# Optimization experiments

Hardware: AMD Instinct MI355X
Metric: run time of the kernel (lower is better)

The kernel has to match this reference:

```python
import jax, jax.numpy as jnp
import numpy as np

N_NODES = 100000
N_EDGES = 1600000
IN_CH = 64
HEADS = 8
OUT_CH = 16
NEG_SLOPE = 0.2  # PyG GATConv default


def setup_inputs() -> dict:
    key = jax.random.key(0)
    ks = jax.random.split(key, 6)
    x = jax.random.normal(ks[0], (N_NODES, IN_CH), dtype=jnp.float32)
    edge_index = jax.random.randint(ks[1], (2, N_EDGES), 0, N_NODES, dtype=jnp.int32)
    # learned parameters (PyG GATConv: shared lin for src/dst, att vectors, bias for concat output)
    W = jax.random.normal(ks[2], (HEADS * OUT_CH, IN_CH), dtype=jnp.float32) / np.sqrt(IN_CH)
    att_src = jax.random.normal(ks[3], (HEADS, OUT_CH), dtype=jnp.float32) / np.sqrt(OUT_CH)
    att_dst = jax.random.normal(ks[4], (HEADS, OUT_CH), dtype=jnp.float32) / np.sqrt(OUT_CH)
    bias = jax.random.normal(ks[5], (HEADS * OUT_CH,), dtype=jnp.float32) * 0.01
    return {"x": x, "edge_index": edge_index, "W": W,
            "att_src": att_src, "att_dst": att_dst, "bias": bias}


def reference(x, edge_index, W, att_src, att_dst, bias):
    n = x.shape[0]
    # linear projection -> [N, H, C]
    h = (x @ W.T).reshape(n, HEADS, OUT_CH)
    # per-node halves of the attention logit
    a_src = jnp.einsum('nhc,hc->nh', h, att_src)  # [N, H]
    a_dst = jnp.einsum('nhc,hc->nh', h, att_dst)  # [N, H]
    # add self loops (PyG default add_self_loops=True)
    loops = jnp.arange(n, dtype=edge_index.dtype)
    src = jnp.concatenate([edge_index[0], loops])
    dst = jnp.concatenate([edge_index[1], loops])
    # edge attention: leaky_relu then segment-softmax over incoming edges of dst
    e = jax.nn.leaky_relu(a_src[src] + a_dst[dst], NEG_SLOPE)  # [E+N, H]
    e_max = jax.ops.segment_max(e, dst, num_segments=n)
    e = jnp.exp(e - e_max[dst])
    denom = jax.ops.segment_sum(e, dst, num_segments=n)
    alpha = e / (denom[dst] + 1e-16)  # [E+N, H]
    # weighted scatter-add aggregation
    msg = h[src] * alpha[:, :, None]  # [E+N, H, C]
    out = jax.ops.segment_sum(msg, dst, num_segments=n).reshape(n, HEADS * OUT_CH)
    out = out + bias
    # unlinear: act='relu', norm=None
    return jax.nn.relu(out)
```

## Files before the change

### kernel.cpp

```cpp
#include <hip/hip_runtime.h>

#define N_NODESC 100000
#define N_EDGESC 1600000
#define HCC 128
#define E_TOTC (N_EDGESC + N_NODESC)
#define SCAN_NB 391
#define PROJ_NB 1563
#define POS_NB 831

using short8 = __attribute__((ext_vector_type(8))) short;
using f32x4  = __attribute__((ext_vector_type(4))) float;

__device__ __forceinline__ float lrelu(float v) { return fmaxf(v, 0.2f * v); }
__device__ __forceinline__ unsigned short f2bf(float f) {
    unsigned u = __float_as_uint(f);
    unsigned r = ((u >> 16) & 1u) + 0x7fffu;
    return (unsigned short)((u + r) >> 16);
}
__device__ __forceinline__ short8 pack8(float4 a, float4 b) {
    short8 v;
    v[0] = (short)f2bf(a.x); v[1] = (short)f2bf(a.y);
    v[2] = (short)f2bf(a.z); v[3] = (short)f2bf(a.w);
    v[4] = (short)f2bf(b.x); v[5] = (short)f2bf(b.y);
    v[6] = (short)f2bf(b.z); v[7] = (short)f2bf(b.w);
    return v;
}

__launch_bounds__(256, 4)
__global__ void proj_pos_kernel(const float* __restrict__ x, const float* __restrict__ W,
                                const float* __restrict__ att_src, const float* __restrict__ att_dst,
                                unsigned short* __restrict__ h16,
                                float* __restrict__ a_src, float* __restrict__ a_dst,
                                const int* __restrict__ ei, int* __restrict__ deg,
                                int* __restrict__ posb) {
    const int t = threadIdx.x;

    if (blockIdx.x >= PROJ_NB) {
        const int e0 = (blockIdx.x - PROJ_NB) * 2048 + t;
#pragma unroll
        for (int j = 0; j < 8; ++j) {
            int e = e0 + 256 * j;
            if (e < E_TOTC) {
                int d = (e < N_EDGESC) ? ei[N_EDGESC + e] : (e - N_EDGESC);
                posb[e] = atomicAdd(&deg[d], 1);
            }
        }
        return;
    }

    const int l  = t & 63;
    const int lc = l & 15;
    const int lg = l >> 4;
    const int row0 = blockIdx.x * 64 + (t >> 6) * 16;
    const int rA = min(row0 + lc, N_NODESC - 1);

    f32x4 acc[8];
#pragma unroll
    for (int i = 0; i < 8; ++i) acc[i] = (f32x4){0.f, 0.f, 0.f, 0.f};

#pragma unroll
    for (int s = 0; s < 2; ++s) {
        const float4* xp = (const float4*)(x + (size_t)rA * 64 + s * 32 + lg * 8);
        float4 x0 = xp[0], x1 = xp[1];
        short8 af = pack8(x0, x1);
#pragma unroll
        for (int t2 = 0; t2 < 8; ++t2) {
            const float4* wp = (const float4*)(W + (size_t)(t2 * 16 + lc) * 64 + s * 32 + lg * 8);
            float4 w0 = wp[0], w1 = wp[1];
            short8 bf = pack8(w0, w1);
            acc[t2] = __builtin_amdgcn_mfma_f32_16x16x32_bf16(af, bf, acc[t2], 0, 0, 0);
        }
    }

#pragma unroll
    for (int hd = 0; hd < 8; ++hd) {
        const float as_ = att_src[hd * 16 + lc];
        const float ad_ = att_dst[hd * 16 + lc];
#pragma unroll
        for (int j = 0; j < 4; ++j) {
            const int grow = row0 + lg * 4 + j;
            const float hv = acc[hd][j];
            float ts = hv * as_;
            float td = hv * ad_;
            ts += __shfl_xor(ts, 1); ts += __shfl_xor(ts, 2);
            ts += __shfl_xor(ts, 4); ts += __shfl_xor(ts, 8);
            td += __shfl_xor(td, 1); td += __shfl_xor(td, 2);
            td += __shfl_xor(td, 4); td += __shfl_xor(td, 8);
            if (grow < N_NODESC) {
                h16[(size_t)grow * HCC + hd * 16 + lc] = f2bf(hv);
                if (lc == 0) {
                    a_src[(size_t)grow * 8 + hd] = ts;
                    a_dst[(size_t)grow * 8 + hd] = td;
                }
            }
        }
    }
}

__global__ void scan1_kernel(const int* __restrict__ deg, int* __restrict__ bsum) {
    __shared__ int lds[256];
    int i = blockIdx.x * 256 + threadIdx.x;
    lds[threadIdx.x] = (i < N_NODESC) ? deg[i] : 0;
    __syncthreads();
    for (int off = 128; off > 0; off >>= 1) {
        if (threadIdx.x < off) lds[threadIdx.x] += lds[threadIdx.x + off];
        __syncthreads();
    }
    if (threadIdx.x == 0) bsum[blockIdx.x] = lds[0];
}

__global__ void scan2_kernel(int* __restrict__ bsum) {
    __shared__ int lds[512];
    int t = threadIdx.x;
    lds[t] = (t < SCAN_NB) ? bsum[t] : 0;
    __syncthreads();
    for (int off = 1; off < 512; off <<= 1) {
        int u = 0;
        if (t >= off) u = lds[t - off];
        __syncthreads();
        if (t >= off) lds[t] += u;
        __syncthreads();
    }
    if (t < SCAN_NB) bsum[t] = (t == 0) ? 0 : lds[t - 1];
}

__global__ void scan3_kernel(const int* __restrict__ deg, const int* __restrict__ bsum,
                             int* __restrict__ rowptr) {
    __shared__ int lds[256];
    int t = threadIdx.x;
    int i = blockIdx.x * 256 + t;
    int v = (i < N_NODESC) ? deg[i] : 0;
    lds[t] = v;
    __syncthreads();
    for (int off = 1; off < 256; off <<= 1) {
        int u = 0;
        if (t >= off) u = lds[t - off];
        __syncthreads();
        if (t >= off) lds[t] += u;
        __syncthreads();
    }
    int excl = bsum[blockIdx.x] + lds[t] - v;
    if (i < N_NODESC) rowptr[i] = excl;
    if (i == 0) rowptr[N_NODESC] = E_TOTC;
}

__global__ void scatter_kernel(const int* __restrict__ ei, const int* __restrict__ rowptr,
                               const int* __restrict__ posb, int* __restrict__ colsrc) {
    int e = blockIdx.x * 256 + threadIdx.x;
    if (e >= E_TOTC) return;
    int s, d;
    if (e < N_EDGESC) { s = ei[e]; d = ei[N_EDGESC + e]; }
    else              { s = d = e - N_EDGESC; }
    colsrc[rowptr[d] + posb[e]] = s;
}

__launch_bounds__(256, 8)
__global__ void agg_csr_kernel(const int* __restrict__ rowptr, const int* __restrict__ colsrc,
                               const float* __restrict__ a_src, const float* __restrict__ a_dst,
                               const unsigned* __restrict__ h32,
                               const float* __restrict__ bias, float* __restrict__ out) {
    const int t = threadIdx.x;
    const int L = t & 63;
    const int n = blockIdx.x * 4 + (t >> 6);
    const int hd = L >> 3;
    const int eL = L & 7;

    const int beg = rowptr[n], end = rowptr[n + 1];
    const float ad = a_dst[n * 8 + hd];

    float den = 0.f;
    float acc[16];
#pragma unroll
    for (int j = 0; j < 16; ++j) acc[j] = 0.f;

    int p = beg + eL;
    bool vld = p < end;
    int s = vld ? colsrc[p] : 0;
    float av = vld ? a_src[s * 8 + hd] : 0.f;

    while (vld) {
        const uint4* hp = (const uint4*)(h32 + (size_t)s * 64 + hd * 8);
        const uint4 ha = hp[0];
        const uint4 hb = hp[1];
        const int p2 = p + 8;
        const bool v2 = p2 < end;
        const int s2 = v2 ? colsrc[p2] : 0;
        const float av2 = v2 ? a_src[s2 * 8 + hd] : 0.f;

        const float pr = __expf(lrelu(av + ad));
        den += pr;
        acc[0]  = fmaf(pr, __uint_as_float(ha.x << 16),         acc[0]);
        acc[1]  = fmaf(pr, __uint_as_float(ha.x & 0xffff0000u), acc[1]);
        acc[2]  = fmaf(pr, __uint_as_float(ha.y << 16),         acc[2]);
        acc[3]  = fmaf(pr, __uint_as_float(ha.y & 0xffff0000u), acc[3]);
        acc[4]  = fmaf(pr, __uint_as_float(ha.z << 16),         acc[4]);
        acc[5]  = fmaf(pr, __uint_as_float(ha.z & 0xffff0000u), acc[5]);
        acc[6]  = fmaf(pr, __uint_as_float(ha.w << 16),         acc[6]);
        acc[7]  = fmaf(pr, __uint_as_float(ha.w & 0xffff0000u), acc[7]);
        acc[8]  = fmaf(pr, __uint_as_float(hb.x << 16),         acc[8]);
        acc[9]  = fmaf(pr, __uint_as_float(hb.x & 0xffff0000u), acc[9]);
        acc[10] = fmaf(pr, __uint_as_float(hb.y << 16),         acc[10]);
        acc[11] = fmaf(pr, __uint_as_float(hb.y & 0xffff0000u), acc[11]);
        acc[12] = fmaf(pr, __uint_as_float(hb.z << 16),         acc[12]);
        acc[13] = fmaf(pr, __uint_as_float(hb.z & 0xffff0000u), acc[13]);
        acc[14] = fmaf(pr, __uint_as_float(hb.w << 16),         acc[14]);
        acc[15] = fmaf(pr, __uint_as_float(hb.w & 0xffff0000u), acc[15]);

        p = p2; s = s2; av = av2; vld = v2;
    }

    den += __shfl_xor(den, 1); den += __shfl_xor(den, 2); den += __shfl_xor(den, 4);
#pragma unroll
    for (int j = 0; j < 16; ++j) {
        acc[j] += __shfl_xor(acc[j], 1);
        acc[j] += __shfl_xor(acc[j], 2);
        acc[j] += __shfl_xor(acc[j], 4);
    }
    const float inv = 1.f / (den + 1e-16f);
    float ox = acc[0], oy = acc[1];
#pragma unroll
    for (int j = 1; j < 8; ++j) {
        ox = (eL == j) ? acc[2 * j]     : ox;
        oy = (eL == j) ? acc[2 * j + 1] : oy;
    }
    const float2 b = ((const float2*)bias)[L];
    float2 o;
    o.x = fmaxf(ox * inv + b.x, 0.f);
    o.y = fmaxf(oy * inv + b.y, 0.f);
    ((float2*)out)[(size_t)n * 64 + L] = o;
}

extern "C" void kernel_launch(void* const* d_in, const int* in_sizes, int n_in,
                              void* d_out, int out_size, void* d_ws, size_t ws_size,
                              hipStream_t stream) {
    const float* x       = (const float*)d_in[0];
    const int*   ei      = (const int*)d_in[1];
    const float* W       = (const float*)d_in[2];
    const float* att_src = (const float*)d_in[3];
    const float* att_dst = (const float*)d_in[4];
    const float* bias    = (const float*)d_in[5];
    float* out = (float*)d_out;

    float* ws    = (float*)d_ws;
    unsigned short* h16 = (unsigned short*)ws;
    float* a_src = ws + 6400000;
    float* a_dst = a_src + 800000;
    int* deg     = (int*)(a_dst + 800000);
    int* rowptr  = deg + 100000;
    int* bsum    = rowptr + 100001;
    int* posb    = bsum + 512;
    int* colsrc  = posb + 1700000;

    hipMemsetAsync(deg, 0, 100000 * sizeof(int), stream);

    proj_pos_kernel<<<PROJ_NB + POS_NB, 256, 0, stream>>>(x, W, att_src, att_dst,
                                                          h16, a_src, a_dst,
                                                          ei, deg, posb);
    scan1_kernel<<<SCAN_NB, 256, 0, stream>>>(deg, bsum);
    scan2_kernel<<<1, 512, 0, stream>>>(bsum);
    scan3_kernel<<<SCAN_NB, 256, 0, stream>>>(deg, bsum, rowptr);
    scatter_kernel<<<(E_TOTC + 255) / 256, 256, 0, stream>>>(ei, rowptr, posb, colsrc);

    agg_csr_kernel<<<N_NODESC / 4, 256, 0, stream>>>(rowptr, colsrc, a_src, a_dst,
                                                     (const unsigned*)h16, bias, out);
}
```

Measured before the change: 226.0 us.

## Replace bf16 MFMA projection with fp32 LDS-tiled GEMM and folded attention vectors

The fused MFMA projection and edge-position kernel is split into three kernels: a small prep kernel that transposes W and folds att_src/att_dst into W to give per-input-channel attention weights, an fp32 LDS-tiled register-blocked projection kernel that computes h and both attention logits directly, and a separate position/atomic kernel. This removes the shuffle reductions and the bf16 rounding of inputs, which improves precision. In exchange it uses fp32 FMA instead of matrix cores, adds two kernel launches, and gives up the overlap between projection and the atomic degree count.

```diff
diff --git a/kernel.cpp b/kernel.cpp
--- a/kernel.cpp
+++ b/kernel.cpp
@@ -5,11 +5,7 @@
 #define HCC 128
 #define E_TOTC (N_EDGESC + N_NODESC)
 #define SCAN_NB 391
-#define PROJ_NB 1563
-#define POS_NB 831
-
-using short8 = __attribute__((ext_vector_type(8))) short;
-using f32x4  = __attribute__((ext_vector_type(4))) float;
+#define PROJ_NB 782
 
 __device__ __forceinline__ float lrelu(float v) { return fmaxf(v, 0.2f * v); }
 __device__ __forceinline__ unsigned short f2bf(float f) {
@@ -17,84 +13,107 @@
     unsigned r = ((u >> 16) & 1u) + 0x7fffu;
     return (unsigned short)((u + r) >> 16);
 }
-__device__ __forceinline__ short8 pack8(float4 a, float4 b) {
-    short8 v;
-    v[0] = (short)f2bf(a.x); v[1] = (short)f2bf(a.y);
-    v[2] = (short)f2bf(a.z); v[3] = (short)f2bf(a.w);
-    v[4] = (short)f2bf(b.x); v[5] = (short)f2bf(b.y);
-    v[6] = (short)f2bf(b.z); v[7] = (short)f2bf(b.w);
-    return v;
-}
-
-__launch_bounds__(256, 4)
-__global__ void proj_pos_kernel(const float* __restrict__ x, const float* __restrict__ W,
-                                const float* __restrict__ att_src, const float* __restrict__ att_dst,
-                                unsigned short* __restrict__ h16,
-                                float* __restrict__ a_src, float* __restrict__ a_dst,
-                                const int* __restrict__ ei, int* __restrict__ deg,
-                                int* __restrict__ posb) {
+
+__global__ void wu_kernel(const float* __restrict__ W,
+                          const float* __restrict__ att_src, const float* __restrict__ att_dst,
+                          float* __restrict__ WT, float* __restrict__ us_g) {
+    int t = blockIdx.x * 256 + threadIdx.x;
+    if (t < 8192) {
+        int k = t >> 7, c = t & 127;
+        WT[t] = W[c * 64 + k];
+    } else {
+        int o = t - 8192;
+        int k = o >> 4, c = o & 15;
+        const int h = (c < 8) ? c : c - 8;
+        const float* av = (c < 8) ? att_src : att_dst;
+        float s = 0.f;
+#pragma unroll
+        for (int j = 0; j < 16; ++j) s += av[h * 16 + j] * W[(h * 16 + j) * 64 + k];
+        us_g[o] = s;
+    }
+}
+
+__launch_bounds__(256, 2)
+__global__ void proj_kernel(const float* __restrict__ x, const float* __restrict__ WT,
+                            const float* __restrict__ us_g,
+                            unsigned short* __restrict__ h16,
+                            float* __restrict__ a_src, float* __restrict__ a_dst) {
+    __shared__ float xs[128][68];
+    __shared__ float ws[64][132];
+    __shared__ float us[64][16];
     const int t = threadIdx.x;
-
-    if (blockIdx.x >= PROJ_NB) {
-        const int e0 = (blockIdx.x - PROJ_NB) * 2048 + t;
-#pragma unroll
-        for (int j = 0; j < 8; ++j) {
-            int e = e0 + 256 * j;
-            if (e < E_TOTC) {
-                int d = (e < N_EDGESC) ? ei[N_EDGESC + e] : (e - N_EDGESC);
-                posb[e] = atomicAdd(&deg[d], 1);
-            }
+    const int row0 = blockIdx.x * 128;
+
+    const float4* wt4 = (const float4*)WT;
+    float4* ws4 = (float4*)&ws[0][0];
+#pragma unroll
+    for (int j = 0; j < 8; ++j) {
+        int q = t + 256 * j;
+        int k = q >> 5, c4 = q & 31;
+        *(float4*)&ws[k][c4 * 4] = wt4[q];
+    }
+    ((float4*)&us[0][0])[t] = ((const float4*)us_g)[t];
+
+#pragma unroll
+    for (int j = 0; j < 8; ++j) {
+        int f = (t + 256 * j) * 4;
+        int r = f >> 6, k = f & 63;
+        int gr = row0 + r;
+        if (gr >= N_NODESC) gr = N_NODESC - 1;
+        float4 v = *(const float4*)&x[(size_t)gr * 64 + k];
+        *(float4*)&xs[r][k] = v;
+    }
+    __syncthreads();
+
+    const int rg = t & 15;
+    const int cg = t >> 4;
+    float acc[8][8], acca[8];
+#pragma unroll
+    for (int i = 0; i < 8; ++i) {
+        acca[i] = 0.f;
+#pragma unroll
+        for (int j = 0; j < 8; ++j) acc[i][j] = 0.f;
+    }
+
+#pragma unroll 4
+    for (int k = 0; k < 64; ++k) {
+        float xv[8];
+#pragma unroll
+        for (int i = 0; i < 8; ++i) xv[i] = xs[rg + 16 * i][k];
+        float4 w0 = *(const float4*)&ws[k][4 * cg];
+        float4 w1 = *(const float4*)&ws[k][64 + 4 * cg];
+        float uv = us[k][cg];
+#pragma unroll
+        for (int i = 0; i < 8; ++i) {
+            acc[i][0] += xv[i] * w0.x; acc[i][1] += xv[i] * w0.y;
+            acc[i][2] += xv[i] * w0.z; acc[i][3] += xv[i] * w0.w;
+            acc[i][4] += xv[i] * w1.x; acc[i][5] += xv[i] * w1.y;
+            acc[i][6] += xv[i] * w1.z; acc[i][7] += xv[i] * w1.w;
+            acca[i]   += xv[i] * uv;
         }
-        return;
-    }
-
-    const int l  = t & 63;
-    const int lc = l & 15;
-    const int lg = l >> 4;
-    const int row0 = blockIdx.x * 64 + (t >> 6) * 16;
-    const int rA = min(row0 + lc, N_NODESC - 1);
-
-    f32x4 acc[8];
-#pragma unroll
-    for (int i = 0; i < 8; ++i) acc[i] = (f32x4){0.f, 0.f, 0.f, 0.f};
-
-#pragma unroll
-    for (int s = 0; s < 2; ++s) {
-        const float4* xp = (const float4*)(x + (size_t)rA * 64 + s * 32 + lg * 8);
-        float4 x0 = xp[0], x1 = xp[1];
-        short8 af = pack8(x0, x1);
-#pragma unroll
-        for (int t2 = 0; t2 < 8; ++t2) {
-            const float4* wp = (const float4*)(W + (size_t)(t2 * 16 + lc) * 64 + s * 32 + lg * 8);
-            float4 w0 = wp[0], w1 = wp[1];
-            short8 bf = pack8(w0, w1);
-            acc[t2] = __builtin_amdgcn_mfma_f32_16x16x32_bf16(af, bf, acc[t2], 0, 0, 0);
+    }
+
+#pragma unroll
+    for (int i = 0; i < 8; ++i) {
+        int gr = row0 + rg + 16 * i;
+        if (gr < N_NODESC) {
+            ushort4 p0, p1;
+            p0.x = f2bf(acc[i][0]); p0.y = f2bf(acc[i][1]); p0.z = f2bf(acc[i][2]); p0.w = f2bf(acc[i][3]);
+            p1.x = f2bf(acc[i][4]); p1.y = f2bf(acc[i][5]); p1.z = f2bf(acc[i][6]); p1.w = f2bf(acc[i][7]);
+            *(ushort4*)&h16[(size_t)gr * HCC + 4 * cg] = p0;
+            *(ushort4*)&h16[(size_t)gr * HCC + 64 + 4 * cg] = p1;
+            if (cg < 8) a_src[(size_t)gr * 8 + cg] = acca[i];
+            else        a_dst[(size_t)gr * 8 + cg - 8] = acca[i];
         }
     }
-
-#pragma unroll
-    for (int hd = 0; hd < 8; ++hd) {
-        const float as_ = att_src[hd * 16 + lc];
-        const float ad_ = att_dst[hd * 16 + lc];
-#pragma unroll
-        for (int j = 0; j < 4; ++j) {
-            const int grow = row0 + lg * 4 + j;
-            const float hv = acc[hd][j];
-            float ts = hv * as_;
-            float td = hv * ad_;
-            ts += __shfl_xor(ts, 1); ts += __shfl_xor(ts, 2);
-            ts += __shfl_xor(ts, 4); ts += __shfl_xor(ts, 8);
-            td += __shfl_xor(td, 1); td += __shfl_xor(td, 2);
-            td += __shfl_xor(td, 4); td += __shfl_xor(td, 8);
-            if (grow < N_NODESC) {
-                h16[(size_t)grow * HCC + hd * 16 + lc] = f2bf(hv);
-                if (lc == 0) {
-                    a_src[(size_t)grow * 8 + hd] = ts;
-                    a_dst[(size_t)grow * 8 + hd] = td;
-                }
-            }
-        }
-    }
+}
+
+__global__ void pos_kernel(const int* __restrict__ ei, int* __restrict__ deg,
+                           int* __restrict__ posb) {
+    int e = blockIdx.x * 256 + threadIdx.x;
+    if (e >= E_TOTC) return;
+    int d = (e < N_EDGESC) ? ei[N_EDGESC + e] : (e - N_EDGESC);
+    posb[e] = atomicAdd(&deg[d], 1);
 }
 
 __global__ void scan1_kernel(const int* __restrict__ deg, int* __restrict__ bsum) {
@@ -245,7 +264,9 @@
     unsigned short* h16 = (unsigned short*)ws;
     float* a_src = ws + 6400000;
     float* a_dst = a_src + 800000;
-    int* deg     = (int*)(a_dst + 800000);
+    float* WT    = a_dst + 800000;
+    float* us_g  = WT + 8192;
+    int* deg     = (int*)(us_g + 1024);
     int* rowptr  = deg + 100000;
     int* bsum    = rowptr + 100001;
     int* posb    = bsum + 512;
@@ -253,9 +274,9 @@
 
     hipMemsetAsync(deg, 0, 100000 * sizeof(int), stream);
 
-    proj_pos_kernel<<<PROJ_NB + POS_NB, 256, 0, stream>>>(x, W, att_src, att_dst,
-                                                          h16, a_src, a_dst,
-                                                          ei, deg, posb);
+    wu_kernel<<<36, 256, 0, stream>>>(W, att_src, att_dst, WT, us_g);
+    proj_kernel<<<PROJ_NB, 256, 0, stream>>>(x, WT, us_g, h16, a_src, a_dst);
+    pos_kernel<<<(E_TOTC + 255) / 256, 256, 0, stream>>>(ei, deg, posb);
     scan1_kernel<<<SCAN_NB, 256, 0, stream>>>(deg, bsum);
     scan2_kernel<<<1, 512, 0, stream>>>(bsum);
     scan3_kernel<<<SCAN_NB, 256, 0, stream>>>(deg, bsum, rowptr);
```

Measured after the change: 230.2 us. About the same (+1.9%).
